# Optimization experiments

Hardware: AMD Instinct MI355X
Metric: run time of the kernel (lower is better)

The kernel has to match this reference:

```python
import jax, jax.numpy as jnp
import numpy as np

EPS = 1e-5
LEAK = 0.01  # PADLoC uses ABN = BatchNorm + LeakyReLU as norm_act


def bn_act(x, g, b):
    # train-mode batch norm over (B,H,W) + leaky relu
    mu = jnp.mean(x, axis=(0, 2, 3), keepdims=True)
    var = jnp.var(x, axis=(0, 2, 3), keepdims=True)
    y = (x - mu) * jax.lax.rsqrt(var + EPS) * g[None, :, None, None] + b[None, :, None, None]
    return jnp.where(y >= 0, y, LEAK * y)


def depthwise3x3(x, w):
    # x: (B,C,H,W), w: (C,1,3,3), dilation (1,1), padding 1, groups=C
    C = x.shape[1]
    return jax.lax.conv_general_dilated(
        x, w, window_strides=(1, 1), padding=((1, 1), (1, 1)),
        feature_group_count=C, dimension_numbers=('NCHW', 'OIHW', 'NCHW'))


def pointwise(x, w):
    # 1x1 conv, no bias; w: (Cout, Cin)
    return jnp.einsum('bchw,oc->bohw', x, w)


def _gather_vals(x_flat, idx):
    # x_flat: (B,C,P), idx: (B,HW,9) float indices -> (B,C,HW,9)
    B, C, P = x_flat.shape
    i = idx.astype(jnp.int32).reshape(B, -1)  # (B, HW*9)
    out = jax.vmap(lambda xf, ii: xf[:, ii])(x_flat, i)  # (B,C,HW*9)
    return out.reshape(B, C, idx.shape[1], 9)


def setup_inputs() -> dict:
    key = jax.random.key(0)
    ks = jax.random.split(key, 8)
    B, Cin, Cout, H, W = 1, 256, 128, 64, 192
    sc = 0.05
    return {
        'x': jax.random.normal(ks[0], (B, Cin, H, W), jnp.float32),
        'x_range': jax.random.normal(ks[1], (B, 1, H, W), jnp.float32),
        'range_out': jax.random.normal(ks[2], (Cin, 1, 3, 3), jnp.float32) * sc,
        'w_reduce': jax.random.normal(ks[3], (Cout, Cin), jnp.float32) * sc,
        'g_r': jnp.ones((Cout,), jnp.float32), 'b_r': jnp.zeros((Cout,), jnp.float32),
        'dw1': jax.random.normal(ks[4], (Cout, 1, 3, 3), jnp.float32) * sc,
        'pw1': jax.random.normal(ks[5], (Cout, Cout), jnp.float32) * sc,
        'g1': jnp.ones((Cout,), jnp.float32), 'b1': jnp.zeros((Cout,), jnp.float32),
        'dw2': jax.random.normal(ks[6], (Cout, 1, 3, 3), jnp.float32) * sc,
        'pw2': jax.random.normal(ks[7], (Cout, Cout), jnp.float32) * sc,
        'g2': jnp.ones((Cout,), jnp.float32), 'b2': jnp.zeros((Cout,), jnp.float32),
    }


def reference(x, x_range, range_out, w_reduce, g_r, b_r, dw1, pw1, g1, b1, dw2, pw2, g2, b2):
    B, Cin, H, W = x.shape
    Hp, Wp = H + 2, W + 2
    P = Hp * Wp  # flattened padded spatial size
    x_off = jnp.array([-1, 0, 1, -1, 0, 1, -1, 0, 1], jnp.float32)
    y_off = jnp.array([-1, -1, -1, 0, 0, 0, 1, 1, 1], jnp.float32)

    offset = 3.0 * jax.nn.sigmoid(x_range)  # (B,1,H,W)

    # base (undeformed) flattened indices of the 9 taps around each interior pixel
    v = jnp.arange(P, dtype=jnp.float32)[:, None]  # (P,1)
    pre_v = v + x_off + y_off * Wp                 # (P,9)
    pre_v = pre_v.reshape(Hp, Wp, 9)[1:H + 1, 1:W + 1].reshape(-1, 9)  # (HW,9)
    pre_v = jnp.broadcast_to(pre_v[None], (B, H * W, 9))

    # fractional offsets: only x-direction is scaled by offset in _3x3box
    offset_v = offset.reshape(B, H * W, 1) * x_off.reshape(1, 1, 9) + (y_off * Wp).reshape(1, 1, 9)

    x_padded = jnp.pad(x, ((0, 0), (0, 0), (1, 1), (1, 1)))  # (B,C,Hp,Wp)
    clamp = lambda a: jnp.clip(a, 0.0, P - 1.0)

    after_v = pre_v + offset_v
    av_f = clamp(pre_v + jnp.floor(offset_v))
    av_f1 = clamp(av_f + x_off)
    av_c = clamp(pre_v + jnp.ceil(offset_v))
    av_c1 = clamp(av_c + x_off)

    xflat = x_padded.reshape(B, Cin, P)
    vf = _gather_vals(xflat, av_f)
    vf1 = _gather_vals(xflat, av_f1)
    vc = _gather_vals(xflat, av_c)
    vc1 = _gather_vals(xflat, av_c1)

    f1 = jnp.abs(after_v - av_f)[:, None] * vf + jnp.abs(av_f1 - after_v)[:, None] * vf1
    f2 = jnp.abs(after_v - av_c1)[:, None] * vc1 + jnp.abs(av_c - after_v)[:, None] * vc
    interp = (jnp.abs((after_v - av_f) / Wp)[:, None] * f1
              + jnp.abs((av_c1 - after_v) / Wp)[:, None] * f2)  # (B,C,HW,9)

    y = jnp.sum(interp * range_out.reshape(1, Cin, 1, 9), -1).reshape(B, Cin, H, W)
    y = bn_act(pointwise(y, w_reduce), g_r, b_r)
    y = bn_act(pointwise(depthwise3x3(y, dw1), pw1), g1, b1)
    y = bn_act(pointwise(depthwise3x3(y, dw2), pw2), g2, b2)
    return y
```

## Files before the change

### kernel.cpp

```cpp
#include <hip/hip_runtime.h>
#include <hip/hip_bf16.h>

#define HW    12288
#define Wimg  192
#define Himg  64
#define Wpad  194
#define Ppad  12804

static __device__ __forceinline__ unsigned short f2bf(float f) {
    union { float f; unsigned int u; } v; v.f = f;
    unsigned int r = v.u + 0x7fffu + ((v.u >> 16) & 1u);
    return (unsigned short)(r >> 16);
}
static __device__ __forceinline__ float bf2f(unsigned short h) {
    union { unsigned int u; float f; } v; v.u = ((unsigned int)h) << 16;
    return v.f;
}
static __device__ __forceinline__ float bflo(unsigned int u) {
    union { unsigned int u; float f; } v; v.u = u << 16; return v.f;
}
static __device__ __forceinline__ float bfhi(unsigned int u) {
    union { unsigned int u; float f; } v; v.u = u & 0xffff0000u; return v.f;
}

__global__ __launch_bounds__(256, 4) void k_deform(
    const float* __restrict__ x,
    const float* __restrict__ xr,
    const float* __restrict__ rout,
    unsigned short* __restrict__ y0)
{
    __shared__ float s_x[32][240];

    const int cblk = blockIdx.x;
    const int tile = blockIdx.y;
    const int tid  = threadIdx.x;
    const int pl   = tid & 63;
    const int wv   = __builtin_amdgcn_readfirstlane(tid >> 6);
    const int h    = tile / 3;
    const int w0   = (tile - h * 3) * 64;
    const int w    = w0 + pl;
    const int gp   = h * Wimg + w;

    int   li[6];
    float gw[6][3];
    const float off = 3.0f / (1.0f + expf(-xr[gp]));

    #pragma unroll
    for (int t = 0; t < 6; ++t) {
        const int xo = (t & 1) ? 1 : -1;
        const int yo = (t >> 1) - 1;
        float ov  = off * (float)xo;
        int   iv  = yo * Wpad;
        int   pre = (h + 1) * Wpad + (w + 1) + xo + iv;
        float after = (float)(pre + iv) + ov;
        int fl = (int)floorf(ov);
        int ce = (int)ceilf(ov);
        int av_f  = min(max(pre + fl + iv, 0), Ppad - 1);
        int av_f1 = min(max(av_f + xo,    0), Ppad - 1);
        int av_c  = min(max(pre + ce + iv, 0), Ppad - 1);
        int av_c1 = min(max(av_c + xo,    0), Ppad - 1);
        float wf  = fabsf(after - (float)av_f);
        float wf1 = fabsf((float)av_f1 - after);
        float wc1 = fabsf(after - (float)av_c1);
        float wc  = fabsf((float)av_c - after);
        float s1 = wf  * (1.0f / Wpad);
        float s2 = wc1 * (1.0f / Wpad);
        int   i4[4] = { av_f, av_f1, av_c1, av_c };
        float w4[4] = { s1 * wf, s1 * wf1, s2 * wc1, s2 * wc };
        int b = min(min(i4[0], i4[1]), min(i4[2], i4[3]));
        const int base = (h + 1 + 2 * yo) * Wpad + w0 - 4;
        li[t] = (t >> 1) * 80 + min(max(b - base, 0), 71);
        #pragma unroll
        for (int s = 0; s < 3; ++s) {
            float ws = 0.0f;
            #pragma unroll
            for (int j = 0; j < 4; ++j)
                ws += (i4[j] == b + s) ? w4[j] : 0.0f;
            int av = b + s;
            int r  = av / Wpad;
            int cc = av - r * Wpad;
            bool inb = (r >= 1) && (r <= Himg) && (cc >= 1) && (cc <= Wimg);
            gw[t][s] = inb ? ws : 0.0f;
        }
    }

    const int jj = tid;
    int  xoff = 0;
    bool valid = false;
    int  rr = 0, jcol = 0;
    if (jj < 222) {
        rr   = jj / 74;
        jcol = jj - rr * 74;
        const int flat = (h + 1 + 2 * (rr - 1)) * Wpad + w0 - 4 + jcol;
        if (flat >= 0 && flat < Ppad) {
            const int r = flat / Wpad;
            const int c = flat - r * Wpad;
            valid = (r >= 1) && (r <= Himg) && (c >= 1) && (c <= Wimg);
            xoff  = valid ? ((r - 1) * Wimg + (c - 1)) : 0;
        }
    }
    const float* xb = x + (size_t)(cblk * 32) * HW;
    for (int c = 0; c < 32; ++c) {
        if (jj < 222) {
            float v = valid ? xb[(size_t)c * HW + xoff] : 0.0f;
            s_x[c][rr * 80 + jcol] = v;
        }
    }
    __syncthreads();

    const int c0l = wv * 8;
    #pragma unroll 2
    for (int i = 0; i < 8; ++i) {
        const int cl = c0l + i;
        const float* sxc = s_x[cl];
        const float* rc  = rout + (cblk * 32 + cl) * 9;
        float acc = 0.0f;
        #pragma unroll
        for (int t = 0; t < 6; ++t) {
            float part = gw[t][0] * sxc[li[t]]
                       + gw[t][1] * sxc[li[t] + 1]
                       + gw[t][2] * sxc[li[t] + 2];
            const int k = 3 * (t >> 1) + ((t & 1) ? 2 : 0);
            acc += rc[k] * part;
        }
        y0[(size_t)(cblk * 32 + cl) * HW + gp] = f2bf(acc);
    }
}

template <int CIN>
__global__ __launch_bounds__(256) void k_pw(
    const unsigned short* __restrict__ A,
    const float* __restrict__ Wm,
    unsigned short* __restrict__ Zp0,
    unsigned short* __restrict__ Zp1)
{
    __shared__ float s_a[32][64];
    __shared__ float s_w[32][68];
    const int tid = threadIdx.x;
    const int tx  = tid & 15;
    const int ty  = tid >> 4;
    const int px0 = blockIdx.x * 64;
    const int o0  = blockIdx.y * 64;
    const int KH  = CIN / 2;
    const int cb0 = blockIdx.z * KH;
    unsigned short* __restrict__ Zp = blockIdx.z ? Zp1 : Zp0;

    float acc[4][4];
    #pragma unroll
    for (int i = 0; i < 4; ++i)
        #pragma unroll
        for (int j = 0; j < 4; ++j) acc[i][j] = 0.0f;

    const int arow = tid >> 3;
    const int acg  = tid & 7;
    const int wo = tid >> 5;
    const int wl = tid & 31;

    for (int cb = cb0; cb < cb0 + KH; cb += 32) {
        {
            const uint4* ap = (const uint4*)(A + (size_t)(cb + arow) * HW + px0);
            uint4 u = ap[acg];
            float4 lo = make_float4(bflo(u.x), bfhi(u.x), bflo(u.y), bfhi(u.y));
            float4 hi = make_float4(bflo(u.z), bfhi(u.z), bflo(u.w), bfhi(u.w));
            *(float4*)&s_a[arow][acg * 8]     = lo;
            *(float4*)&s_a[arow][acg * 8 + 4] = hi;
        }
        #pragma unroll
        for (int i = 0; i < 8; ++i)
            s_w[wl][wo + 8 * i] = Wm[(size_t)(o0 + wo + 8 * i) * CIN + cb + wl];
        __syncthreads();
        #pragma unroll
        for (int cc = 0; cc < 32; ++cc) {
            float4 a4 = *(const float4*)&s_a[cc][tx * 4];
            float4 w4 = *(const float4*)&s_w[cc][ty * 4];
            acc[0][0] += w4.x * a4.x; acc[0][1] += w4.x * a4.y;
            acc[0][2] += w4.x * a4.z; acc[0][3] += w4.x * a4.w;
            acc[1][0] += w4.y * a4.x; acc[1][1] += w4.y * a4.y;
            acc[1][2] += w4.y * a4.z; acc[1][3] += w4.y * a4.w;
            acc[2][0] += w4.z * a4.x; acc[2][1] += w4.z * a4.y;
            acc[2][2] += w4.z * a4.z; acc[2][3] += w4.z * a4.w;
            acc[3][0] += w4.w * a4.x; acc[3][1] += w4.w * a4.y;
            acc[3][2] += w4.w * a4.z; acc[3][3] += w4.w * a4.w;
        }
        __syncthreads();
    }

    #pragma unroll
    for (int i = 0; i < 4; ++i) {
        ushort4 v;
        v.x = f2bf(acc[i][0]); v.y = f2bf(acc[i][1]);
        v.z = f2bf(acc[i][2]); v.w = f2bf(acc[i][3]);
        *(ushort4*)&Zp[(size_t)(o0 + ty * 4 + i) * HW + px0 + tx * 4] = v;
    }
}

__global__ __launch_bounds__(256) void k_combine(
    const unsigned short* __restrict__ Zp0,
    const unsigned short* __restrict__ Zp1,
    unsigned short* __restrict__ Z,
    float* __restrict__ psum)
{
    __shared__ float s_s[4], s_q[4];
    const int c   = blockIdx.x >> 2;
    const int seg = blockIdx.x & 3;
    const int tid = threadIdx.x;
    const size_t base = (size_t)c * HW + seg * 3072;
    const uint2* a4 = (const uint2*)(Zp0 + base);
    const uint2* b4 = (const uint2*)(Zp1 + base);
    ushort4*     z4 = (ushort4*)(Z + base);
    float s = 0.0f, q = 0.0f;
    #pragma unroll
    for (int i = 0; i < 3; ++i) {
        uint2 a = a4[tid + i * 256];
        uint2 b = b4[tid + i * 256];
        float v0 = bflo(a.x) + bflo(b.x);
        float v1 = bfhi(a.x) + bfhi(b.x);
        float v2 = bflo(a.y) + bflo(b.y);
        float v3 = bfhi(a.y) + bfhi(b.y);
        ushort4 zz; zz.x = f2bf(v0); zz.y = f2bf(v1);
        zz.z = f2bf(v2); zz.w = f2bf(v3);
        z4[tid + i * 256] = zz;
        s += v0 + v1 + v2 + v3;
        q += v0 * v0 + v1 * v1 + v2 * v2 + v3 * v3;
    }
    #pragma unroll
    for (int off = 32; off > 0; off >>= 1) {
        s += __shfl_down(s, off, 64);
        q += __shfl_down(q, off, 64);
    }
    if ((tid & 63) == 0) { s_s[tid >> 6] = s; s_q[tid >> 6] = q; }
    __syncthreads();
    if (tid == 0) {
        s = s_s[0] + s_s[1] + s_s[2] + s_s[3];
        q = s_q[0] + s_q[1] + s_q[2] + s_q[3];
        atomicAdd(&psum[2 * c],     s);
        atomicAdd(&psum[2 * c + 1], q);
    }
}

__global__ __launch_bounds__(256) void k_dw(
    const unsigned short* __restrict__ Z,
    const float* __restrict__ psum,
    const float* __restrict__ g,
    const float* __restrict__ b,
    const float* __restrict__ dwgt,
    ushort4* __restrict__ D)
{
    const int t  = blockIdx.x * 256 + threadIdx.x;
    const int c  = t / 3072;
    const int gg = t - c * 3072;
    const int h  = gg / 48;
    const int w0 = (gg - h * 48) << 2;

    const float s   = psum[2 * c];
    const float q   = psum[2 * c + 1];
    const float mu  = s * (1.0f / HW);
    const float var = q * (1.0f / HW) - mu * mu;
    const float sc  = g[c] * rsqrtf(var + 1e-5f);
    const float sh  = b[c] - mu * sc;

    float wk[9];
    #pragma unroll
    for (int k = 0; k < 9; ++k) wk[k] = dwgt[c * 9 + k];

    const unsigned short* zc = Z + (size_t)c * HW;
    float v[3][6];
    #pragma unroll
    for (int ky = 0; ky < 3; ++ky) {
        const int hh  = h + ky - 1;
        const bool rin = (hh >= 0) && (hh < Himg);
        #pragma unroll
        for (int j = 0; j < 6; ++j) {
            const int ww = w0 - 1 + j;
            const bool in = rin && (ww >= 0) && (ww < Wimg);
            float z = in ? bf2f(zc[hh * Wimg + ww]) : 0.0f;
            float y = z * sc + sh;
            y = (y >= 0.0f) ? y : 0.01f * y;
            v[ky][j] = in ? y : 0.0f;
        }
    }

    ushort4 o;
    float oo[4];
    #pragma unroll
    for (int j = 0; j < 4; ++j) {
        float a = 0.0f;
        #pragma unroll
        for (int ky = 0; ky < 3; ++ky)
            #pragma unroll
            for (int kx = 0; kx < 3; ++kx)
                a += wk[ky * 3 + kx] * v[ky][j + kx];
        oo[j] = a;
    }
    o.x = f2bf(oo[0]); o.y = f2bf(oo[1]); o.z = f2bf(oo[2]); o.w = f2bf(oo[3]);
    D[t] = o;
}

__global__ __launch_bounds__(256) void k_final(
    const unsigned short* __restrict__ Z,
    const float* __restrict__ psum,
    const float* __restrict__ g,
    const float* __restrict__ b,
    float4* __restrict__ out)
{
    const int f = blockIdx.x * 256 + threadIdx.x;
    const int c = f / 3072;

    const float s   = psum[2 * c];
    const float q   = psum[2 * c + 1];
    const float mu  = s * (1.0f / HW);
    const float var = q * (1.0f / HW) - mu * mu;
    const float sc  = g[c] * rsqrtf(var + 1e-5f);
    const float sh  = b[c] - mu * sc;

    uint2 zz = ((const uint2*)Z)[f];
    float4 v;
    v.x = bflo(zz.x) * sc + sh; v.x = (v.x >= 0.0f) ? v.x : 0.01f * v.x;
    v.y = bfhi(zz.x) * sc + sh; v.y = (v.y >= 0.0f) ? v.y : 0.01f * v.y;
    v.z = bflo(zz.y) * sc + sh; v.z = (v.z >= 0.0f) ? v.z : 0.01f * v.z;
    v.w = bfhi(zz.y) * sc + sh; v.w = (v.w >= 0.0f) ? v.w : 0.01f * v.w;
    out[f] = v;
}

extern "C" void kernel_launch(void* const* d_in, const int* in_sizes, int n_in,
                              void* d_out, int out_size, void* d_ws, size_t ws_size,
                              hipStream_t stream) {
    const float* x   = (const float*)d_in[0];
    const float* xr  = (const float*)d_in[1];
    const float* ro  = (const float*)d_in[2];
    const float* wr  = (const float*)d_in[3];
    const float* gr  = (const float*)d_in[4];
    const float* br  = (const float*)d_in[5];
    const float* dw1 = (const float*)d_in[6];
    const float* pw1 = (const float*)d_in[7];
    const float* g1  = (const float*)d_in[8];
    const float* b1  = (const float*)d_in[9];
    const float* dw2 = (const float*)d_in[10];
    const float* pw2 = (const float*)d_in[11];
    const float* g2  = (const float*)d_in[12];
    const float* b2  = (const float*)d_in[13];

    unsigned short* WS = (unsigned short*)d_ws;
    unsigned short* y0  = WS;
    unsigned short* zlo = WS;
    unsigned short* zhi = WS + 1572864;
    unsigned short* B   = WS + 6291456;
    unsigned short* C   = WS + 9437184;
    float* p1 = (float*)(WS + 12582912);
    float* p2 = p1 + 256;
    float* p3 = p2 + 256;
    float* out = (float*)d_out;

    hipMemsetAsync(p1, 0, 768 * 4, stream);

    k_deform<<<dim3(8, 192), 256, 0, stream>>>(x, xr, ro, y0);
    k_pw<256><<<dim3(192, 2, 2), 256, 0, stream>>>(y0, wr, B, C);
    k_combine<<<512, 256, 0, stream>>>(B, C, zlo, p1);
    k_dw<<<1536, 256, 0, stream>>>(zlo, p1, gr, br, dw1, (ushort4*)zhi);
    k_pw<128><<<dim3(192, 2, 2), 256, 0, stream>>>(zhi, pw1, B, C);
    k_combine<<<512, 256, 0, stream>>>(B, C, zlo, p2);
    k_dw<<<1536, 256, 0, stream>>>(zlo, p2, g1, b1, dw2, (ushort4*)zhi);
    k_pw<128><<<dim3(192, 2, 2), 256, 0, stream>>>(zhi, pw2, B, C);
    k_combine<<<512, 256, 0, stream>>>(B, C, zlo, p3);
    k_final<<<1536, 256, 0, stream>>>(zlo, p3, g2, b2, (float4*)out);
}
```

Before: 176.1 us.

## Fuse BN+depthwise into pointwise GEMM and drop the combine writeback

The separate combine and depthwise kernels are replaced. The stats kernel now only reduces the two split-K partial buffers into BN sums and writes no combined tensor. A new fused kernel reads both partials, applies BN+LeakyReLU and the 3x3 depthwise conv in shared memory per 64-pixel row tile, then runs the 128x128 pointwise GEMM directly, and the final kernel sums the partials itself. This removes two kernel launches and several full-tensor round trips, but each block now recomputes depthwise halos for its output-channel half (blockIdx.y), which duplicates input reads and depthwise work and raises shared memory use.

```diff
diff --git a/kernel.cpp b/kernel.cpp
--- a/kernel.cpp
+++ b/kernel.cpp
@@ -194,10 +194,9 @@
     }
 }
 
-__global__ __launch_bounds__(256) void k_combine(
+__global__ __launch_bounds__(256) void k_stats(
     const unsigned short* __restrict__ Zp0,
     const unsigned short* __restrict__ Zp1,
-    unsigned short* __restrict__ Z,
     float* __restrict__ psum)
 {
     __shared__ float s_s[4], s_q[4];
@@ -207,7 +206,6 @@
     const size_t base = (size_t)c * HW + seg * 3072;
     const uint2* a4 = (const uint2*)(Zp0 + base);
     const uint2* b4 = (const uint2*)(Zp1 + base);
-    ushort4*     z4 = (ushort4*)(Z + base);
     float s = 0.0f, q = 0.0f;
     #pragma unroll
     for (int i = 0; i < 3; ++i) {
@@ -217,9 +215,6 @@
         float v1 = bfhi(a.x) + bfhi(b.x);
         float v2 = bflo(a.y) + bflo(b.y);
         float v3 = bfhi(a.y) + bfhi(b.y);
-        ushort4 zz; zz.x = f2bf(v0); zz.y = f2bf(v1);
-        zz.z = f2bf(v2); zz.w = f2bf(v3);
-        z4[tid + i * 256] = zz;
         s += v0 + v1 + v2 + v3;
         q += v0 * v0 + v1 * v1 + v2 * v2 + v3 * v3;
     }
@@ -238,66 +233,133 @@
     }
 }
 
-__global__ __launch_bounds__(256) void k_dw(
-    const unsigned short* __restrict__ Z,
+__global__ __launch_bounds__(256) void k_pwdw(
+    const unsigned short* __restrict__ Zp0,
+    const unsigned short* __restrict__ Zp1,
     const float* __restrict__ psum,
     const float* __restrict__ g,
     const float* __restrict__ b,
     const float* __restrict__ dwgt,
-    ushort4* __restrict__ D)
+    const float* __restrict__ Wm,
+    unsigned short* __restrict__ Zq0,
+    unsigned short* __restrict__ Zq1)
 {
-    const int t  = blockIdx.x * 256 + threadIdx.x;
-    const int c  = t / 3072;
-    const int gg = t - c * 3072;
-    const int h  = gg / 48;
-    const int w0 = (gg - h * 48) << 2;
-
-    const float s   = psum[2 * c];
-    const float q   = psum[2 * c + 1];
-    const float mu  = s * (1.0f / HW);
-    const float var = q * (1.0f / HW) - mu * mu;
-    const float sc  = g[c] * rsqrtf(var + 1e-5f);
-    const float sh  = b[c] - mu * sc;
-
-    float wk[9];
-    #pragma unroll
-    for (int k = 0; k < 9; ++k) wk[k] = dwgt[c * 9 + k];
-
-    const unsigned short* zc = Z + (size_t)c * HW;
-    float v[3][6];
-    #pragma unroll
-    for (int ky = 0; ky < 3; ++ky) {
-        const int hh  = h + ky - 1;
-        const bool rin = (hh >= 0) && (hh < Himg);
-        #pragma unroll
-        for (int j = 0; j < 6; ++j) {
-            const int ww = w0 - 1 + j;
-            const bool in = rin && (ww >= 0) && (ww < Wimg);
-            float z = in ? bf2f(zc[hh * Wimg + ww]) : 0.0f;
-            float y = z * sc + sh;
-            y = (y >= 0.0f) ? y : 0.01f * y;
-            v[ky][j] = in ? y : 0.0f;
-        }
-    }
-
-    ushort4 o;
-    float oo[4];
-    #pragma unroll
-    for (int j = 0; j < 4; ++j) {
-        float a = 0.0f;
-        #pragma unroll
-        for (int ky = 0; ky < 3; ++ky)
+    __shared__ float s_z[3][32][68];
+    __shared__ float s_a[32][68];
+    __shared__ float s_w[32][68];
+    __shared__ float s_sc[64], s_sh[64];
+
+    const int tid = threadIdx.x;
+    const int tx  = tid & 15;
+    const int ty  = tid >> 4;
+    const int h   = blockIdx.x / 3;
+    const int w0  = (blockIdx.x - h * 3) * 64;
+    const int px0 = h * Wimg + w0;
+    const int o0  = blockIdx.y * 64;
+    const int bz  = blockIdx.z;
+    unsigned short* __restrict__ Zq = bz ? Zq1 : Zq0;
+
+    if (tid < 64) {
+        const int ci = bz * 64 + tid;
+        const float s  = psum[2 * ci];
+        const float q  = psum[2 * ci + 1];
+        const float mu = s * (1.0f / HW);
+        const float var = q * (1.0f / HW) - mu * mu;
+        const float sc = g[ci] * rsqrtf(var + 1e-5f);
+        s_sc[tid] = sc;
+        s_sh[tid] = b[ci] - mu * sc;
+    }
+    __syncthreads();
+
+    float acc[4][4];
+    #pragma unroll
+    for (int i = 0; i < 4; ++i)
+        #pragma unroll
+        for (int j = 0; j < 4; ++j) acc[i][j] = 0.0f;
+
+    const int wo = tid >> 5;
+    const int wl = tid & 31;
+
+    for (int ck = 0; ck < 2; ++ck) {
+        const int cl0 = ck * 32;
+        #pragma unroll
+        for (int j = 0; j < 26; ++j) {
+            const int idx = tid + j * 256;
+            if (idx < 6528) {
+                const int r   = idx / 2176;
+                const int rem = idx - r * 2176;
+                const int c   = rem / 68;
+                const int col = rem - c * 68;
+                float y = 0.0f;
+                if (col < 66) {
+                    const int grow = h - 1 + r;
+                    const int gcol = w0 - 1 + col;
+                    if (grow >= 0 && grow < Himg && gcol >= 0 && gcol < Wimg) {
+                        const int ci = bz * 64 + cl0 + c;
+                        const size_t off = (size_t)ci * HW + grow * Wimg + gcol;
+                        float z = bf2f(Zp0[off]) + bf2f(Zp1[off]);
+                        y = z * s_sc[cl0 + c] + s_sh[cl0 + c];
+                        y = (y >= 0.0f) ? y : 0.01f * y;
+                    }
+                }
+                s_z[r][c][col] = y;
+            }
+        }
+        #pragma unroll
+        for (int i = 0; i < 8; ++i)
+            s_w[wl][wo + 8 * i] =
+                Wm[(size_t)(o0 + wo + 8 * i) * 128 + bz * 64 + cl0 + wl];
+        __syncthreads();
+
+        {
+            const int c  = tid >> 3;
+            const int p0 = tid & 7;
+            const int ci = bz * 64 + cl0 + c;
+            float wk[9];
             #pragma unroll
-            for (int kx = 0; kx < 3; ++kx)
-                a += wk[ky * 3 + kx] * v[ky][j + kx];
-        oo[j] = a;
-    }
-    o.x = f2bf(oo[0]); o.y = f2bf(oo[1]); o.z = f2bf(oo[2]); o.w = f2bf(oo[3]);
-    D[t] = o;
-}
-
-__global__ __launch_bounds__(256) void k_final(
-    const unsigned short* __restrict__ Z,
+            for (int k = 0; k < 9; ++k) wk[k] = dwgt[ci * 9 + k];
+            #pragma unroll
+            for (int k = 0; k < 8; ++k) {
+                const int px = p0 + 8 * k;
+                float a = 0.0f;
+                #pragma unroll
+                for (int ky = 0; ky < 3; ++ky)
+                    #pragma unroll
+                    for (int kx = 0; kx < 3; ++kx)
+                        a += wk[ky * 3 + kx] * s_z[ky][c][px + kx];
+                s_a[c][px] = a;
+            }
+        }
+        __syncthreads();
+
+        #pragma unroll
+        for (int cc = 0; cc < 32; ++cc) {
+            float4 a4 = *(const float4*)&s_a[cc][tx * 4];
+            float4 w4 = *(const float4*)&s_w[cc][ty * 4];
+            acc[0][0] += w4.x * a4.x; acc[0][1] += w4.x * a4.y;
+            acc[0][2] += w4.x * a4.z; acc[0][3] += w4.x * a4.w;
+            acc[1][0] += w4.y * a4.x; acc[1][1] += w4.y * a4.y;
+            acc[1][2] += w4.y * a4.z; acc[1][3] += w4.y * a4.w;
+            acc[2][0] += w4.z * a4.x; acc[2][1] += w4.z * a4.y;
+            acc[2][2] += w4.z * a4.z; acc[2][3] += w4.z * a4.w;
+            acc[3][0] += w4.w * a4.x; acc[3][1] += w4.w * a4.y;
+            acc[3][2] += w4.w * a4.z; acc[3][3] += w4.w * a4.w;
+        }
+        __syncthreads();
+    }
+
+    #pragma unroll
+    for (int i = 0; i < 4; ++i) {
+        ushort4 v;
+        v.x = f2bf(acc[i][0]); v.y = f2bf(acc[i][1]);
+        v.z = f2bf(acc[i][2]); v.w = f2bf(acc[i][3]);
+        *(ushort4*)&Zq[(size_t)(o0 + ty * 4 + i) * HW + px0 + tx * 4] = v;
+    }
+}
+
+__global__ __launch_bounds__(256) void k_final2(
+    const unsigned short* __restrict__ Zp0,
+    const unsigned short* __restrict__ Zp1,
     const float* __restrict__ psum,
     const float* __restrict__ g,
     const float* __restrict__ b,
@@ -313,12 +375,13 @@
     const float sc  = g[c] * rsqrtf(var + 1e-5f);
     const float sh  = b[c] - mu * sc;
 
-    uint2 zz = ((const uint2*)Z)[f];
+    uint2 a = ((const uint2*)Zp0)[f];
+    uint2 d = ((const uint2*)Zp1)[f];
     float4 v;
-    v.x = bflo(zz.x) * sc + sh; v.x = (v.x >= 0.0f) ? v.x : 0.01f * v.x;
-    v.y = bfhi(zz.x) * sc + sh; v.y = (v.y >= 0.0f) ? v.y : 0.01f * v.y;
-    v.z = bflo(zz.y) * sc + sh; v.z = (v.z >= 0.0f) ? v.z : 0.01f * v.z;
-    v.w = bfhi(zz.y) * sc + sh; v.w = (v.w >= 0.0f) ? v.w : 0.01f * v.w;
+    v.x = (bflo(a.x) + bflo(d.x)) * sc + sh; v.x = (v.x >= 0.0f) ? v.x : 0.01f * v.x;
+    v.y = (bfhi(a.x) + bfhi(d.x)) * sc + sh; v.y = (v.y >= 0.0f) ? v.y : 0.01f * v.y;
+    v.z = (bflo(a.y) + bflo(d.y)) * sc + sh; v.z = (v.z >= 0.0f) ? v.z : 0.01f * v.z;
+    v.w = (bfhi(a.y) + bfhi(d.y)) * sc + sh; v.w = (v.w >= 0.0f) ? v.w : 0.01f * v.w;
     out[f] = v;
 }
 
@@ -342,11 +405,11 @@
 
     unsigned short* WS = (unsigned short*)d_ws;
     unsigned short* y0  = WS;
-    unsigned short* zlo = WS;
-    unsigned short* zhi = WS + 1572864;
-    unsigned short* B   = WS + 6291456;
-    unsigned short* C   = WS + 9437184;
-    float* p1 = (float*)(WS + 12582912);
+    unsigned short* P0a = WS + 3145728;
+    unsigned short* P0b = WS + 4718592;
+    unsigned short* P1a = WS + 6291456;
+    unsigned short* P1b = WS + 7864320;
+    float* p1 = (float*)(WS + 9437184);
     float* p2 = p1 + 256;
     float* p3 = p2 + 256;
     float* out = (float*)d_out;
@@ -354,13 +417,13 @@
     hipMemsetAsync(p1, 0, 768 * 4, stream);
 
     k_deform<<<dim3(8, 192), 256, 0, stream>>>(x, xr, ro, y0);
-    k_pw<256><<<dim3(192, 2, 2), 256, 0, stream>>>(y0, wr, B, C);
-    k_combine<<<512, 256, 0, stream>>>(B, C, zlo, p1);
-    k_dw<<<1536, 256, 0, stream>>>(zlo, p1, gr, br, dw1, (ushort4*)zhi);
-    k_pw<128><<<dim3(192, 2, 2), 256, 0, stream>>>(zhi, pw1, B, C);
-    k_combine<<<512, 256, 0, stream>>>(B, C, zlo, p2);
-    k_dw<<<1536, 256, 0, stream>>>(zlo, p2, g1, b1, dw2, (ushort4*)zhi);
-    k_pw<128><<<dim3(192, 2, 2), 256, 0, stream>>>(zhi, pw2, B, C);
-    k_combine<<<512, 256, 0, stream>>>(B, C, zlo, p3);
-    k_final<<<1536, 256, 0, stream>>>(zlo, p3, g2, b2, (float4*)out);
-}
+    k_pw<256><<<dim3(192, 2, 2), 256, 0, stream>>>(y0, wr, P0a, P0b);
+    k_stats<<<512, 256, 0, stream>>>(P0a, P0b, p1);
+    k_pwdw<<<dim3(192, 2, 2), 256, 0, stream>>>(P0a, P0b, p1, gr, br, dw1, pw1,
+                                                P1a, P1b);
+    k_stats<<<512, 256, 0, stream>>>(P1a, P1b, p2);
+    k_pwdw<<<dim3(192, 2, 2), 256, 0, stream>>>(P1a, P1b, p2, g1, b1, dw2, pw2,
+                                                P0a, P0b);
+    k_stats<<<512, 256, 0, stream>>>(P0a, P0b, p3);
+    k_final2<<<1536, 256, 0, stream>>>(P0a, P0b, p3, g2, b2, (float4*)out);
+}
```

Result: slower. 267.9 us (+52.1%).
